# Performance work log

Measured on AMD Instinct MI355X. Metric: run time of the kernel, lower is better.

## Reference

```python
import jax, jax.numpy as jnp
import numpy as np

DENS = 0.016355
N = 2048
DIM = 3
BATCH = 8
L = (N / DENS) ** (1.0 / 3.0)  # periodic box length ~50.03
B_DECAY, M_POW = 2.6, 5.0      # backflow decay fn params


def _backflow(x):
    # x: (n, dim) particle positions
    n = x.shape[0]
    x = x - L * jnp.floor(x / L)                      # wrap into box [0, L)
    rij = x[:, None, :] - x[None, :, :]               # (n, n, dim)
    rij = rij - L * jnp.rint(rij / L)                 # minimum-image convention
    dij = jnp.linalg.norm(rij, axis=-1)               # (n, n)
    eye = jnp.eye(n, dtype=bool)
    # original masks out self-pairs (i==j); emulate with safe divide + zero weight
    dij_safe = jnp.where(eye, 1.0, dij)
    fr = 0.5 * (jnp.exp(-((B_DECAY / dij_safe) ** M_POW)) - 1.0)
    fr = jnp.where(eye, 0.0, fr)                      # (n, n), zero on diagonal
    return x + jnp.einsum('ij,ijd->id', fr, rij)      # backflow-shifted coords


def setup_inputs() -> dict:
    key = jax.random.key(0)
    # positions uniform in the periodic box
    x = jax.random.uniform(key, (BATCH, N, DIM), dtype=jnp.float32) * jnp.float32(L)
    return {"x": x}


def reference(x) -> jnp.ndarray:
    # x: (batch, n, dim) -> (batch, n, dim)
    return jax.vmap(_backflow)(x)
```

## Files before the change

### kernel.cpp

```cpp
#include <hip/hip_runtime.h>
#include <math.h>

#define NPART 2048
#define NDIM  3
#define IPB   16
#define SPLIT 16
#define BLOCK (IPB * SPLIT)

__global__ __launch_bounds__(BLOCK, 4)
void backflow_kernel(const float* __restrict__ x, float* __restrict__ out,
                     float L, float invL) {
    __shared__ float xs[NPART];
    __shared__ float ys[NPART];
    __shared__ float zs[NPART];

    const int tid   = threadIdx.x;
    const int blk   = blockIdx.x;
    const int b     = blk >> 7;
    const int ibase = (blk & 127) * IPB;
    const float* xb = x + b * (NPART * NDIM);

    for (int e = tid; e < NPART * NDIM; e += BLOCK) {
        float v = xb[e];
        v = v - L * floorf(v * invL);
        int p = e / 3;
        int c = e - 3 * p;
        if      (c == 0) xs[p] = v;
        else if (c == 1) ys[p] = v;
        else             zs[p] = v;
    }
    __syncthreads();

    const int sub = tid & (SPLIT - 1);
    const int ii  = tid >> 4;
    const int i   = ibase + ii;

    const float xi = xs[i];
    const float yi = ys[i];
    const float zi = zs[i];

    float ax = 0.0f, ay = 0.0f, az = 0.0f;

    #pragma unroll 4
    for (int k = 0; k < NPART / SPLIT; ++k) {
        const int j = sub + k * SPLIT;
        float dx = xi - xs[j];
        float dy = yi - ys[j];
        float dz = zi - zs[j];
        dx = fmaf(-L, rintf(dx * invL), dx);
        dy = fmaf(-L, rintf(dy * invL), dy);
        dz = fmaf(-L, rintf(dz * invL), dz);
        float d2 = fmaf(dx, dx, fmaf(dy, dy, dz * dz));
        float rinv = rsqrtf(d2);
        float t  = 2.6f * rinv;
        float t2 = t * t;
        float t5 = t2 * t2 * t;
        float fr = fmaf(0.5f, __expf(-t5), -0.5f);
        ax = fmaf(fr, dx, ax);
        ay = fmaf(fr, dy, ay);
        az = fmaf(fr, dz, az);
    }

    #pragma unroll
    for (int off = 8; off >= 1; off >>= 1) {
        ax += __shfl_xor(ax, off);
        ay += __shfl_xor(ay, off);
        az += __shfl_xor(az, off);
    }

    if (sub == 0) {
        float* o = out + (b * NPART + i) * NDIM;
        o[0] = xi + ax;
        o[1] = yi + ay;
        o[2] = zi + az;
    }
}

extern "C" void kernel_launch(void* const* d_in, const int* in_sizes, int n_in,
                              void* d_out, int out_size, void* d_ws, size_t ws_size,
                              hipStream_t stream) {
    (void)in_sizes; (void)n_in; (void)d_ws; (void)ws_size; (void)out_size;
    const float* x = (const float*)d_in[0];
    float* out     = (float*)d_out;

    const double Ld = cbrt(2048.0 / 0.016355);
    const float  L    = (float)Ld;
    const float  invL = (float)(1.0 / Ld);

    const int nblocks = (8 * NPART) / IPB;
    backflow_kernel<<<nblocks, BLOCK, 0, stream>>>(x, out, L, invL);
}
```

Measured before the change: 83.61 us.

## Work in box-normalized coordinates with float4 LDS and exp2 constant folding

Positions are rescaled by 1/L so the minimum-image step becomes a plain subtract of rint, and the wrap and output are scaled back by L. The decay exponent folds 2.6^5/L^5·log2(e) into one constant so a single exp2 and rsq intrinsic handle the pair weight. Particles are stored as float4 in LDS for one vector load per pair, and the split per particle grows from 16 to 32 lanes with a higher occupancy hint. This trims ALU work per pair, at the cost of a larger LDS footprint and a small change in float rounding.

New measurement: 72.44 us. -13.4%, faster.

```diff
diff --git a/kernel.cpp b/kernel.cpp
--- a/kernel.cpp
+++ b/kernel.cpp
@@ -2,77 +2,85 @@
 #include <math.h>
 
 #define NPART 2048
-#define NDIM  3
 #define IPB   16
-#define SPLIT 16
+#define SPLIT 32
 #define BLOCK (IPB * SPLIT)
 
-__global__ __launch_bounds__(BLOCK, 4)
+#if __has_builtin(__builtin_amdgcn_rsqf)
+#define RSQF(x) __builtin_amdgcn_rsqf(x)
+#else
+#define RSQF(x) rsqrtf(x)
+#endif
+#if __has_builtin(__builtin_amdgcn_exp2f)
+#define EXP2F(x) __builtin_amdgcn_exp2f(x)
+#else
+#define EXP2F(x) exp2f(x)
+#endif
+
+__global__ __launch_bounds__(BLOCK, 8)
 void backflow_kernel(const float* __restrict__ x, float* __restrict__ out,
-                     float L, float invL) {
-    __shared__ float xs[NPART];
-    __shared__ float ys[NPART];
-    __shared__ float zs[NPART];
+                     float L, float invL, float K) {
+    __shared__ float4 ps[NPART];
 
     const int tid   = threadIdx.x;
     const int blk   = blockIdx.x;
     const int b     = blk >> 7;
     const int ibase = (blk & 127) * IPB;
-    const float* xb = x + b * (NPART * NDIM);
+    const float* xb = x + b * (NPART * 3);
 
-    for (int e = tid; e < NPART * NDIM; e += BLOCK) {
-        float v = xb[e];
-        v = v - L * floorf(v * invL);
-        int p = e / 3;
-        int c = e - 3 * p;
-        if      (c == 0) xs[p] = v;
-        else if (c == 1) ys[p] = v;
-        else             zs[p] = v;
+    for (int p = tid; p < NPART; p += BLOCK) {
+        float ux = xb[3 * p + 0] * invL;
+        float uy = xb[3 * p + 1] * invL;
+        float uz = xb[3 * p + 2] * invL;
+        ux -= floorf(ux);
+        uy -= floorf(uy);
+        uz -= floorf(uz);
+        ps[p] = make_float4(ux, uy, uz, 0.0f);
     }
     __syncthreads();
 
     const int sub = tid & (SPLIT - 1);
-    const int ii  = tid >> 4;
+    const int ii  = tid >> 5;
     const int i   = ibase + ii;
 
-    const float xi = xs[i];
-    const float yi = ys[i];
-    const float zi = zs[i];
+    const float4 pi = ps[i];
+    const float uxi = pi.x, uyi = pi.y, uzi = pi.z;
 
     float ax = 0.0f, ay = 0.0f, az = 0.0f;
 
     #pragma unroll 4
     for (int k = 0; k < NPART / SPLIT; ++k) {
-        const int j = sub + k * SPLIT;
-        float dx = xi - xs[j];
-        float dy = yi - ys[j];
-        float dz = zi - zs[j];
-        dx = fmaf(-L, rintf(dx * invL), dx);
-        dy = fmaf(-L, rintf(dy * invL), dy);
-        dz = fmaf(-L, rintf(dz * invL), dz);
-        float d2 = fmaf(dx, dx, fmaf(dy, dy, dz * dz));
-        float rinv = rsqrtf(d2);
-        float t  = 2.6f * rinv;
-        float t2 = t * t;
-        float t5 = t2 * t2 * t;
-        float fr = fmaf(0.5f, __expf(-t5), -0.5f);
+        const int j = sub + (k << 5);
+        const float4 pj = ps[j];
+        float dx = uxi - pj.x;
+        float dy = uyi - pj.y;
+        float dz = uzi - pj.z;
+        dx -= rintf(dx);
+        dy -= rintf(dy);
+        dz -= rintf(dz);
+        float d2  = fmaf(dx, dx, fmaf(dy, dy, dz * dz));
+        float ri  = RSQF(d2);
+        float ri2 = ri * ri;
+        float ri4 = ri2 * ri2;
+        float e   = EXP2F((K * ri4) * ri);
+        float fr  = fmaf(0.5f, e, -0.5f);
         ax = fmaf(fr, dx, ax);
         ay = fmaf(fr, dy, ay);
         az = fmaf(fr, dz, az);
     }
 
     #pragma unroll
-    for (int off = 8; off >= 1; off >>= 1) {
+    for (int off = 16; off >= 1; off >>= 1) {
         ax += __shfl_xor(ax, off);
         ay += __shfl_xor(ay, off);
         az += __shfl_xor(az, off);
     }
 
     if (sub == 0) {
-        float* o = out + (b * NPART + i) * NDIM;
-        o[0] = xi + ax;
-        o[1] = yi + ay;
-        o[2] = zi + az;
+        float* o = out + (b * NPART + i) * 3;
+        o[0] = L * (uxi + ax);
+        o[1] = L * (uyi + ay);
+        o[2] = L * (uzi + az);
     }
 }
 
@@ -83,10 +91,13 @@
     const float* x = (const float*)d_in[0];
     float* out     = (float*)d_out;
 
-    const double Ld = cbrt(2048.0 / 0.016355);
+    const double Ld   = cbrt(2048.0 / 0.016355);
+    const double t    = 2.6 / Ld;
+    const double Kd   = -(t * t * t * t * t) * 1.4426950408889634;
     const float  L    = (float)Ld;
     const float  invL = (float)(1.0 / Ld);
+    const float  K    = (float)Kd;
 
     const int nblocks = (8 * NPART) / IPB;
-    backflow_kernel<<<nblocks, BLOCK, 0, stream>>>(x, out, L, invL);
+    backflow_kernel<<<nblocks, BLOCK, 0, stream>>>(x, out, L, invL, K);
 }
```
